# Performance work log

Measured on AMD Instinct MI355X. Metric: run time of the kernel, lower is better.

## Reference

```python
import jax, jax.numpy as jnp
import numpy as np

N, E = 50000, 800000
D_IN, D_E = 256, 64
H1, H2 = 128, 128
N_OUT = 64
LEAKY_SLOPE = 0.01  # torch.nn.LeakyReLU default
EPS = 1e-16         # PyG softmax denominator eps


def setup_inputs() -> dict:
    key = jax.random.key(0)
    ks = jax.random.split(key, 32)

    def w(k, shape, s=0.05):
        return jax.random.normal(k, shape, dtype=jnp.float32) * s

    inp = {
        "x_in": jax.random.normal(ks[0], (N, D_IN), dtype=jnp.float32),
        "edge_index": jax.random.randint(ks[1], (2, E), 0, N),
        "edge_atts": jax.random.normal(ks[2], (E, D_E), dtype=jnp.float32),
        # TransformerConv layer 1 (in=D_IN, out=H1, heads=1, beta=True, edge_dim=D_E)
        "Wq1": w(ks[3], (H1, D_IN)), "bq1": jnp.zeros((H1,), jnp.float32),
        "Wk1": w(ks[4], (H1, D_IN)), "bk1": jnp.zeros((H1,), jnp.float32),
        "Wv1": w(ks[5], (H1, D_IN)), "bv1": jnp.zeros((H1,), jnp.float32),
        "We1": w(ks[6], (H1, D_E)),                     # lin_edge (bias=False)
        "Wskip1": w(ks[7], (H1, D_IN)), "bskip1": jnp.zeros((H1,), jnp.float32),
        "Wbeta1": w(ks[8], (1, 3 * H1)),                # lin_beta (bias=False)
        # TransformerConv layer 2 (in=H1, out=H2)
        "Wq2": w(ks[9], (H2, H1)), "bq2": jnp.zeros((H2,), jnp.float32),
        "Wk2": w(ks[10], (H2, H1)), "bk2": jnp.zeros((H2,), jnp.float32),
        "Wv2": w(ks[11], (H2, H1)), "bv2": jnp.zeros((H2,), jnp.float32),
        "We2": w(ks[12], (H2, D_E)),
        "Wskip2": w(ks[13], (H2, H1)), "bskip2": jnp.zeros((H2,), jnp.float32),
        "Wbeta2": w(ks[14], (1, 3 * H2)),
        # output MLP: Linear(H1 + H2 -> N_OUT)
        "Wm": w(ks[15], (N_OUT, H1 + H2)), "bm": jnp.zeros((N_OUT,), jnp.float32),
    }
    return inp


def _transformer_conv(x, src, dst, edge_attr,
                      Wq, bq, Wk, bk, Wv, bv, We, Wskip, bskip, Wbeta, n_nodes):
    """PyG TransformerConv: heads=1, concat=True, beta=True, root_weight=True,
    dropout inactive (eval mode)."""
    d = Wq.shape[0]
    q = x @ Wq.T + bq                      # [N, d]
    k = x @ Wk.T + bk                      # [N, d]
    v = x @ Wv.T + bv                      # [N, d]
    e = edge_attr @ We.T                   # [E, d]
    k_e = k[src] + e                       # gather source keys + edge embedding
    v_e = v[src] + e                       # gather source values + edge embedding
    # attention score per edge
    score = jnp.einsum('ed,ed->e', q[dst], k_e) / jnp.sqrt(jnp.asarray(d, jnp.float32))
    # segment softmax over incoming edges of each destination node
    m = jax.ops.segment_max(score, dst, num_segments=n_nodes)
    m = jnp.where(jnp.isfinite(m), m, 0.0)
    ex = jnp.exp(score - m[dst])
    denom = jax.ops.segment_sum(ex, dst, num_segments=n_nodes) + EPS
    alpha = ex / denom[dst]                # [E]
    # scatter-add weighted messages
    out = jax.ops.segment_sum(alpha[:, None] * v_e, dst, num_segments=n_nodes)  # [N, d]
    # beta-gated skip connection
    x_r = x @ Wskip.T + bskip
    beta = jax.nn.sigmoid(jnp.concatenate([out, x_r, out - x_r], axis=1) @ Wbeta.T)  # [N, 1]
    return beta * x_r + (1.0 - beta) * out


def _leaky_relu(x):
    return jnp.where(x >= 0, x, LEAKY_SLOPE * x)


def reference(x_in, edge_index, edge_atts,
              Wq1, bq1, Wk1, bk1, Wv1, bv1, We1, Wskip1, bskip1, Wbeta1,
              Wq2, bq2, Wk2, bk2, Wv2, bv2, We2, Wskip2, bskip2, Wbeta2,
              Wm, bm):
    src, dst = edge_index[0], edge_index[1]
    n = x_in.shape[0]
    x1 = _leaky_relu(_transformer_conv(x_in, src, dst, edge_atts,
                                       Wq1, bq1, Wk1, bk1, Wv1, bv1, We1,
                                       Wskip1, bskip1, Wbeta1, n))
    x2 = _leaky_relu(_transformer_conv(x1, src, dst, edge_atts,
                                       Wq2, bq2, Wk2, bk2, Wv2, bv2, We2,
                                       Wskip2, bskip2, Wbeta2, n))
    out = jnp.concatenate([x1, x2], axis=1) @ Wm.T + bm   # [N, N_OUT]
    return out
```

## Files before the change

kernel.cpp:

```cpp
#include <hip/hip_runtime.h>
#include <hip/hip_bf16.h>
#include <math.h>


__global__ void count_deg(const int* __restrict__ dst, int* __restrict__ cnt, int E) {
    int e = blockIdx.x * blockDim.x + threadIdx.x;
    if (e < E) atomicAdd(&cnt[dst[e]], 1);
}

__global__ __launch_bounds__(1024) void scan_a(const int* __restrict__ cnt,
                                               int* __restrict__ out,
                                               int* __restrict__ partials, int N) {
    __shared__ int sh[1024];
    int tid = threadIdx.x;
    int gid = blockIdx.x * 1024 + tid;
    int v = (gid < N) ? cnt[gid] : 0;
    sh[tid] = v;
    for (int off = 1; off < 1024; off <<= 1) {
        __syncthreads();
        int add = (tid >= off) ? sh[tid - off] : 0;
        __syncthreads();
        sh[tid] += add;
    }
    __syncthreads();
    if (gid <= N) out[gid] = sh[tid] - v;
    if (tid == 1023) partials[blockIdx.x] = sh[1023];
}

__global__ void scan_b(int* __restrict__ partials, int nb) {
    if (threadIdx.x == 0 && blockIdx.x == 0) {
        int run = 0;
        for (int i = 0; i < nb; ++i) { int t = partials[i]; partials[i] = run; run += t; }
    }
}

__global__ __launch_bounds__(1024) void scan_c(int* __restrict__ out,
                                               const int* __restrict__ partials,
                                               int* __restrict__ fillb, int N) {
    int gid = blockIdx.x * 1024 + threadIdx.x;
    if (gid <= N) {
        int v = out[gid] + partials[blockIdx.x];
        out[gid] = v;
        fillb[gid] = v;
    }
}

__global__ void fill_edges(const int* __restrict__ src, const int* __restrict__ dst,
                           int* __restrict__ fillb, int2* __restrict__ esi, int E) {
    int e = blockIdx.x * blockDim.x + threadIdx.x;
    if (e < E) {
        int d = dst[e];
        int slot = atomicAdd(&fillb[d], 1);
        esi[slot] = make_int2(src[e], e);
    }
}

__global__ void transpose_we(const float* __restrict__ We, float* __restrict__ WeT) {
    int i = blockIdx.x * blockDim.x + threadIdx.x;
    if (i < 128 * 64) {
        int r = i >> 6, c = i & 63;
        WeT[c * 128 + r] = We[i];
    }
}

__global__ void build_wcat(const float* __restrict__ Wq, const float* __restrict__ Wk,
                           const float* __restrict__ Wv, const float* __restrict__ Ws,
                           const float* __restrict__ bq, const float* __restrict__ bk,
                           const float* __restrict__ bv, const float* __restrict__ bs,
                           float* __restrict__ Wcat, float* __restrict__ bcat,
                           int K, int kshift) {
    int i = blockIdx.x * blockDim.x + threadIdx.x;
    int total = 512 * K;
    if (i < total) {
        int r = i >> kshift;
        float v;
        if (r < 128)      v = Wq[i];
        else if (r < 256) v = Wk[i - (128 << kshift)];
        else if (r < 384) v = Wv[i - (256 << kshift)];
        else              v = Ws[i - (384 << kshift)];
        Wcat[i] = v;
    }
    if (i < 128) {
        bcat[i]       = bq[i];
        bcat[128 + i] = bk[i];
        bcat[256 + i] = bv[i];
        bcat[384 + i] = bs[i];
    }
}

#define TM 128
#define TO 64
#define TKK 16
__global__ __launch_bounds__(256) void gemm_nt2(const float* __restrict__ X, int ldx,
                                                const float* __restrict__ W,
                                                const float* __restrict__ bias,
                                                float* __restrict__ Out, int ldo,
                                                int Nrows, int K) {
    __shared__ float Xs[TKK][TM];
    __shared__ float Ws[TKK][TO];
    int n0 = blockIdx.x * TM, o0 = blockIdx.y * TO;
    int t  = threadIdx.x;
    int tx = t & 15, ty = t >> 4;
    int lr = t >> 1, lk = (t & 1) * 8;
    int wr = t >> 2, wk = (t & 3) * 4;
    float acc[8][4] = {};
    for (int k0 = 0; k0 < K; k0 += TKK) {
        int gr = n0 + lr;
        float4 x0 = make_float4(0.f, 0.f, 0.f, 0.f);
        float4 x1 = make_float4(0.f, 0.f, 0.f, 0.f);
        if (gr < Nrows) {
            const float* xp = &X[(size_t)gr * ldx + k0 + lk];
            x0 = *reinterpret_cast<const float4*>(xp);
            x1 = *reinterpret_cast<const float4*>(xp + 4);
        }
        Xs[lk + 0][lr] = x0.x; Xs[lk + 1][lr] = x0.y;
        Xs[lk + 2][lr] = x0.z; Xs[lk + 3][lr] = x0.w;
        Xs[lk + 4][lr] = x1.x; Xs[lk + 5][lr] = x1.y;
        Xs[lk + 6][lr] = x1.z; Xs[lk + 7][lr] = x1.w;
        float4 wv = *reinterpret_cast<const float4*>(&W[(size_t)(o0 + wr) * K + k0 + wk]);
        Ws[wk + 0][wr] = wv.x; Ws[wk + 1][wr] = wv.y;
        Ws[wk + 2][wr] = wv.z; Ws[wk + 3][wr] = wv.w;
        __syncthreads();
#pragma unroll
        for (int k = 0; k < TKK; ++k) {
            float4 a0 = *reinterpret_cast<const float4*>(&Xs[k][ty * 8]);
            float4 a1 = *reinterpret_cast<const float4*>(&Xs[k][ty * 8 + 4]);
            float4 b  = *reinterpret_cast<const float4*>(&Ws[k][tx * 4]);
            float av_[8] = {a0.x, a0.y, a0.z, a0.w, a1.x, a1.y, a1.z, a1.w};
            float bv_[4] = {b.x, b.y, b.z, b.w};
#pragma unroll
            for (int i = 0; i < 8; ++i)
#pragma unroll
                for (int j = 0; j < 4; ++j)
                    acc[i][j] = fmaf(av_[i], bv_[j], acc[i][j]);
        }
        __syncthreads();
    }
#pragma unroll
    for (int i = 0; i < 8; ++i) {
        int r = n0 + ty * 8 + i;
        if (r < Nrows) {
            int oc = o0 + tx * 4;
            float4 o4;
            o4.x = acc[i][0]; o4.y = acc[i][1]; o4.z = acc[i][2]; o4.w = acc[i][3];
            if (bias) {
                o4.x += bias[oc + 0]; o4.y += bias[oc + 1];
                o4.z += bias[oc + 2]; o4.w += bias[oc + 3];
            }
            *reinterpret_cast<float4*>(&Out[(size_t)r * ldo + oc]) = o4;
        }
    }
}

#define AW3 4
__global__ __launch_bounds__(256) void attn3(
    const int* __restrict__ row_ptr, const int2* __restrict__ esi,
    const float* __restrict__ QKVS, const float* __restrict__ QE,
    const float* __restrict__ Ae, float* __restrict__ Acc, int Nn) {
    int t = threadIdx.x;
    int wid = t >> 6, lane = t & 63;
    const float RS = 0.088388347648318447f;
    for (int n = blockIdx.x * AW3 + wid; n < Nn; n += gridDim.x * AW3) {
        int r0 = row_ptr[n], r1 = row_ptr[n + 1];
        const float* qrow = QKVS + (size_t)n * 512;
        float q0  = qrow[lane];
        float q1  = qrow[64 + lane];
        float qe0 = QE[(size_t)n * 64 + lane];
        float m = -1e30f, l = 0.f, av0 = 0.f, av1 = 0.f, aa = 0.f;
        for (int p = r0; p < r1; p += 8) {
            int pi[8];
#pragma unroll
            for (int i = 0; i < 8; ++i) pi[i] = (p + i < r1) ? p + i : r1 - 1;
            int2 se[8];
#pragma unroll
            for (int i = 0; i < 8; ++i) se[i] = esi[pi[i]];
            float k0v[8], k1v[8], a0v[8];
#pragma unroll
            for (int i = 0; i < 8; ++i) {
                const float* kr = QKVS + (size_t)se[i].x * 512 + 128;
                k0v[i] = kr[lane]; k1v[i] = kr[64 + lane];
            }
#pragma unroll
            for (int i = 0; i < 8; ++i) a0v[i] = Ae[(size_t)se[i].y * 64 + lane];
            float d[8];
#pragma unroll
            for (int i = 0; i < 8; ++i)
                d[i] = fmaf(q0, k0v[i], fmaf(q1, k1v[i], qe0 * a0v[i]));
#pragma unroll
            for (int off = 32; off; off >>= 1) {
#pragma unroll
                for (int i = 0; i < 8; ++i) d[i] += __shfl_xor(d[i], off, 64);
            }
            float v0v[8], v1v[8];
#pragma unroll
            for (int i = 0; i < 8; ++i) {
                const float* vr = QKVS + (size_t)se[i].x * 512 + 256;
                v0v[i] = vr[lane]; v1v[i] = vr[64 + lane];
            }
            float sc[8];
#pragma unroll
            for (int i = 0; i < 8; ++i) sc[i] = (p + i < r1) ? d[i] * RS : -1e30f;
            float bm = sc[0];
#pragma unroll
            for (int i = 1; i < 8; ++i) bm = fmaxf(bm, sc[i]);
            float mn = fmaxf(m, bm);
            float scale = __expf(m - mn);
            float w[8];
#pragma unroll
            for (int i = 0; i < 8; ++i) w[i] = __expf(sc[i] - mn);
            float ws = ((w[0] + w[1]) + (w[2] + w[3])) + ((w[4] + w[5]) + (w[6] + w[7]));
            l = fmaf(l, scale, ws);
            float s_aa = 0.f, s0 = 0.f, s1 = 0.f;
#pragma unroll
            for (int i = 0; i < 8; ++i) {
                s_aa = fmaf(w[i], a0v[i], s_aa);
                s0   = fmaf(w[i], v0v[i], s0);
                s1   = fmaf(w[i], v1v[i], s1);
            }
            aa  = fmaf(aa,  scale, s_aa);
            av0 = fmaf(av0, scale, s0);
            av1 = fmaf(av1, scale, s1);
            m = mn;
        }
        float inv = 1.0f / (l + 1e-16f);
        float* arow = Acc + (size_t)n * 192;
        arow[lane]       = av0 * inv;
        arow[64 + lane]  = av1 * inv;
        arow[128 + lane] = aa * inv;
    }
}

__global__ __launch_bounds__(256) void epilogue_k(
    const float* __restrict__ Acc, const float* __restrict__ QKVS,
    const float* __restrict__ WeT, const float* __restrict__ Wbeta,
    float* __restrict__ Xout, int ldo, int Nn) {
    __shared__ float WeS[64 * 128];
    __shared__ float wbA[128], wbB[128];
    int t = threadIdx.x;
    for (int i = t; i < 64 * 128; i += 256) WeS[i] = WeT[i];
    if (t < 128) {
        float w3 = Wbeta[256 + t];
        wbA[t] = Wbeta[t] + w3;
        wbB[t] = Wbeta[128 + t] - w3;
    }
    __syncthreads();
    int wid = t >> 6, lane = t & 63;
    for (int n = blockIdx.x * 4 + wid; n < Nn; n += gridDim.x * 4) {
        const float* ar = Acc + (size_t)n * 192;
        float out0 = ar[lane], out1 = ar[64 + lane], aa = ar[128 + lane];
#pragma unroll
        for (int j = 0; j < 64; ++j) {
            float aj = __shfl(aa, j, 64);
            out0 = fmaf(aj, WeS[j * 128 + lane], out0);
            out1 = fmaf(aj, WeS[j * 128 + 64 + lane], out1);
        }
        const float* qrow = QKVS + (size_t)n * 512;
        float xr0 = qrow[384 + lane], xr1 = qrow[448 + lane];
        float bp = wbA[lane] * out0 + wbA[64 + lane] * out1 +
                   wbB[lane] * xr0  + wbB[64 + lane] * xr1;
#pragma unroll
        for (int off = 32; off; off >>= 1) bp += __shfl_xor(bp, off, 64);
        float beta = 1.0f / (1.0f + __expf(-bp));
        float x0 = beta * xr0 + (1.0f - beta) * out0;
        float x1 = beta * xr1 + (1.0f - beta) * out1;
        x0 = (x0 >= 0.f) ? x0 : 0.01f * x0;
        x1 = (x1 >= 0.f) ? x1 : 0.01f * x1;
        Xout[(size_t)n * ldo + lane]      = x0;
        Xout[(size_t)n * ldo + 64 + lane] = x1;
    }
}

extern "C" void kernel_launch(void* const* d_in, const int* in_sizes, int n_in,
                              void* d_out, int out_size, void* d_ws, size_t ws_size,
                              hipStream_t stream) {
    const float* x_in  = (const float*)d_in[0];
    const int*   eidx  = (const int*)d_in[1];
    const float* eatt  = (const float*)d_in[2];
    const float* Wq1 = (const float*)d_in[3];  const float* bq1 = (const float*)d_in[4];
    const float* Wk1 = (const float*)d_in[5];  const float* bk1 = (const float*)d_in[6];
    const float* Wv1 = (const float*)d_in[7];  const float* bv1 = (const float*)d_in[8];
    const float* We1 = (const float*)d_in[9];
    const float* Wskip1 = (const float*)d_in[10]; const float* bskip1 = (const float*)d_in[11];
    const float* Wbeta1 = (const float*)d_in[12];
    const float* Wq2 = (const float*)d_in[13]; const float* bq2 = (const float*)d_in[14];
    const float* Wk2 = (const float*)d_in[15]; const float* bk2 = (const float*)d_in[16];
    const float* Wv2 = (const float*)d_in[17]; const float* bv2 = (const float*)d_in[18];
    const float* We2 = (const float*)d_in[19];
    const float* Wskip2 = (const float*)d_in[20]; const float* bskip2 = (const float*)d_in[21];
    const float* Wbeta2 = (const float*)d_in[22];
    const float* Wm  = (const float*)d_in[23]; const float* bm  = (const float*)d_in[24];

    const int N = in_sizes[0] / 256;
    const int E = in_sizes[1] / 2;
    const int* srcp = eidx;
    const int* dstp = eidx + E;

    char* p = (char*)d_ws;
    auto alloc = [&](size_t bytes) -> void* {
        void* r = (void*)p;
        p += (bytes + 255) & ~(size_t)255;
        return r;
    };
    int*   row_ptr  = (int*)alloc((size_t)(N + 1) * 4);
    int*   fillb    = (int*)alloc((size_t)(N + 1) * 4);
    int*   partials = (int*)alloc(256 * 4);
    int2*  esi      = (int2*)alloc((size_t)E * 8);
    float* QKVS = (float*)alloc((size_t)N * 512 * 4);
    float* QEb  = (float*)alloc((size_t)N * 64 * 4);
    float* Accb = (float*)alloc((size_t)N * 192 * 4);
    float* xcat = (float*)alloc((size_t)N * 256 * 4);
    float* WeT  = (float*)alloc((size_t)64 * 128 * 4);
    float* Wcat = (float*)alloc((size_t)512 * 256 * 4);
    float* bcat = (float*)alloc((size_t)512 * 4);

    hipMemsetAsync(fillb, 0, (size_t)(N + 1) * 4, stream);
    count_deg<<<(E + 255) / 256, 256, 0, stream>>>(dstp, fillb, E);
    int nScanBlocks = (N + 1 + 1023) / 1024;
    scan_a<<<nScanBlocks, 1024, 0, stream>>>(fillb, row_ptr, partials, N);
    scan_b<<<1, 1, 0, stream>>>(partials, nScanBlocks);
    scan_c<<<nScanBlocks, 1024, 0, stream>>>(row_ptr, partials, fillb, N);
    fill_edges<<<(E + 255) / 256, 256, 0, stream>>>(srcp, dstp, fillb, esi, E);

    dim3 blk(256);
    int gx = (N + TM - 1) / TM;

    build_wcat<<<(512 * 256 + 255) / 256, 256, 0, stream>>>(
        Wq1, Wk1, Wv1, Wskip1, bq1, bk1, bv1, bskip1, Wcat, bcat, 256, 8);
    transpose_we<<<(128 * 64 + 255) / 256, 256, 0, stream>>>(We1, WeT);
    gemm_nt2<<<dim3(gx, 8), blk, 0, stream>>>(x_in, 256, Wcat, bcat, QKVS, 512, N, 256);
    gemm_nt2<<<dim3(gx, 1), blk, 0, stream>>>(QKVS, 512, WeT, nullptr, QEb, 64, N, 128);
    attn3<<<2048, blk, 0, stream>>>(row_ptr, esi, QKVS, QEb, eatt, Accb, N);
    epilogue_k<<<1024, blk, 0, stream>>>(Accb, QKVS, WeT, Wbeta1, xcat, 256, N);

    build_wcat<<<(512 * 128 + 255) / 256, 256, 0, stream>>>(
        Wq2, Wk2, Wv2, Wskip2, bq2, bk2, bv2, bskip2, Wcat, bcat, 128, 7);
    transpose_we<<<(128 * 64 + 255) / 256, 256, 0, stream>>>(We2, WeT);
    gemm_nt2<<<dim3(gx, 8), blk, 0, stream>>>(xcat, 256, Wcat, bcat, QKVS, 512, N, 128);
    gemm_nt2<<<dim3(gx, 1), blk, 0, stream>>>(QKVS, 512, WeT, nullptr, QEb, 64, N, 128);
    attn3<<<2048, blk, 0, stream>>>(row_ptr, esi, QKVS, QEb, eatt, Accb, N);
    epilogue_k<<<1024, blk, 0, stream>>>(Accb, QKVS, WeT, Wbeta2, xcat + 128, 256, N);

    gemm_nt2<<<dim3(gx, 1), blk, 0, stream>>>(xcat, 256, Wm, bm, (float*)d_out, 64, N, 256);
}
```

Before: 1.145 ms.

## Use split-bf16 MFMA GEMMs and fold the q·We projection into the QKVS GEMM

Replaces the fp32 FMA tiled GEMM with an MFMA kernel that splits each operand into bf16 high and low planes and sums three products, keeping close to fp32 accuracy on matrix cores. It also precomputes We·Wq so the query-edge projection comes out of the main GEMM as 64 extra output columns, removing the separate second GEMM and its buffer. Layer outputs are written directly as bf16 hi/lo planes for the next GEMM. The cost is three MFMAs per tile instead of one, extra split kernels, and a small change in rounding.

```diff
diff --git a/kernel.cpp b/kernel.cpp
--- a/kernel.cpp
+++ b/kernel.cpp
@@ -2,6 +2,21 @@
 #include <hip/hip_bf16.h>
 #include <math.h>
 
+typedef unsigned short u16;
+typedef __attribute__((ext_vector_type(8))) short bf16x8;
+typedef __attribute__((ext_vector_type(4))) float f32x4;
+
+__device__ inline u16 f2bf(float x) {
+    unsigned u = __float_as_uint(x);
+    unsigned r = u + 0x7fff + ((u >> 16) & 1);
+    return (u16)(r >> 16);
+}
+__device__ inline float bf2f(u16 h) { return __uint_as_float(((unsigned)h) << 16); }
+__device__ inline void bsplit(float x, u16& h, u16& l) {
+    h = f2bf(x);
+    float r = x - bf2f(h);
+    l = f2bf(r);
+}
 
 __global__ void count_deg(const int* __restrict__ dst, int* __restrict__ cnt, int E) {
     int e = blockIdx.x * blockDim.x + threadIdx.x;
@@ -63,21 +78,40 @@
     }
 }
 
+__global__ __launch_bounds__(256) void wcomb_k(const float* __restrict__ We,
+                                               const float* __restrict__ Wq,
+                                               const float* __restrict__ bq,
+                                               float* __restrict__ WcT,
+                                               float* __restrict__ bqe, int Din) {
+    int o = blockIdx.x;
+    int d = threadIdx.x;
+    float s = 0.f, sb = 0.f;
+    for (int h = 0; h < 128; ++h) {
+        float w = We[h * 64 + o];
+        if (d < Din) s = fmaf(w, Wq[h * Din + d], s);
+        sb = fmaf(w, bq[h], sb);
+    }
+    if (d < Din) WcT[o * Din + d] = s;
+    if (d == 0) bqe[o] = sb;
+}
+
 __global__ void build_wcat(const float* __restrict__ Wq, const float* __restrict__ Wk,
                            const float* __restrict__ Wv, const float* __restrict__ Ws,
+                           const float* __restrict__ Wc,
                            const float* __restrict__ bq, const float* __restrict__ bk,
                            const float* __restrict__ bv, const float* __restrict__ bs,
+                           const float* __restrict__ bqe,
                            float* __restrict__ Wcat, float* __restrict__ bcat,
                            int K, int kshift) {
     int i = blockIdx.x * blockDim.x + threadIdx.x;
-    int total = 512 * K;
-    if (i < total) {
+    if (i < 576 * K) {
         int r = i >> kshift;
         float v;
         if (r < 128)      v = Wq[i];
         else if (r < 256) v = Wk[i - (128 << kshift)];
         else if (r < 384) v = Wv[i - (256 << kshift)];
-        else              v = Ws[i - (384 << kshift)];
+        else if (r < 512) v = Ws[i - (384 << kshift)];
+        else              v = Wc[i - (512 << kshift)];
         Wcat[i] = v;
     }
     if (i < 128) {
@@ -86,86 +120,121 @@
         bcat[256 + i] = bv[i];
         bcat[384 + i] = bs[i];
     }
-}
-
-#define TM 128
-#define TO 64
-#define TKK 16
-__global__ __launch_bounds__(256) void gemm_nt2(const float* __restrict__ X, int ldx,
-                                                const float* __restrict__ W,
-                                                const float* __restrict__ bias,
-                                                float* __restrict__ Out, int ldo,
-                                                int Nrows, int K) {
-    __shared__ float Xs[TKK][TM];
-    __shared__ float Ws[TKK][TO];
-    int n0 = blockIdx.x * TM, o0 = blockIdx.y * TO;
-    int t  = threadIdx.x;
-    int tx = t & 15, ty = t >> 4;
-    int lr = t >> 1, lk = (t & 1) * 8;
-    int wr = t >> 2, wk = (t & 3) * 4;
-    float acc[8][4] = {};
-    for (int k0 = 0; k0 < K; k0 += TKK) {
-        int gr = n0 + lr;
-        float4 x0 = make_float4(0.f, 0.f, 0.f, 0.f);
-        float4 x1 = make_float4(0.f, 0.f, 0.f, 0.f);
-        if (gr < Nrows) {
-            const float* xp = &X[(size_t)gr * ldx + k0 + lk];
-            x0 = *reinterpret_cast<const float4*>(xp);
-            x1 = *reinterpret_cast<const float4*>(xp + 4);
-        }
-        Xs[lk + 0][lr] = x0.x; Xs[lk + 1][lr] = x0.y;
-        Xs[lk + 2][lr] = x0.z; Xs[lk + 3][lr] = x0.w;
-        Xs[lk + 4][lr] = x1.x; Xs[lk + 5][lr] = x1.y;
-        Xs[lk + 6][lr] = x1.z; Xs[lk + 7][lr] = x1.w;
-        float4 wv = *reinterpret_cast<const float4*>(&W[(size_t)(o0 + wr) * K + k0 + wk]);
-        Ws[wk + 0][wr] = wv.x; Ws[wk + 1][wr] = wv.y;
-        Ws[wk + 2][wr] = wv.z; Ws[wk + 3][wr] = wv.w;
+    if (i < 64) bcat[512 + i] = bqe[i];
+}
+
+__global__ void split_planes(const float* __restrict__ src, u16* __restrict__ hi,
+                             u16* __restrict__ lo, int n4) {
+    int i = (blockIdx.x * blockDim.x + threadIdx.x) * 4;
+    if (i < n4) {
+        float4 v = *reinterpret_cast<const float4*>(&src[i]);
+        u16 h0, h1, h2, h3, l0, l1, l2, l3;
+        bsplit(v.x, h0, l0); bsplit(v.y, h1, l1);
+        bsplit(v.z, h2, l2); bsplit(v.w, h3, l3);
+        ushort4 hv = make_ushort4(h0, h1, h2, h3);
+        ushort4 lv = make_ushort4(l0, l1, l2, l3);
+        *reinterpret_cast<ushort4*>(&hi[i]) = hv;
+        *reinterpret_cast<ushort4*>(&lo[i]) = lv;
+    }
+}
+
+#define BM 128
+#define BO 64
+#define BKX 64
+#define LSTR 72
+__global__ __launch_bounds__(256) void gemm_mfma(
+    const u16* __restrict__ XH, const u16* __restrict__ XL, int ldx,
+    const u16* __restrict__ WH, const u16* __restrict__ WL,
+    const float* __restrict__ bias, float* __restrict__ Out, int ldo,
+    int Nrows, int K) {
+    __shared__ __align__(16) u16 XsH[BM * LSTR];
+    __shared__ __align__(16) u16 XsL[BM * LSTR];
+    __shared__ __align__(16) u16 WsH[BO * LSTR];
+    __shared__ __align__(16) u16 WsL[BO * LSTR];
+    int n0 = blockIdx.x * BM, o0 = blockIdx.y * BO;
+    int t = threadIdx.x, wid = t >> 6, lane = t & 63;
+    int xr = t >> 1, xk = (t & 1) * 32;
+    int wr = t >> 2, wk = (t & 3) * 16;
+    bool xok = (n0 + xr) < Nrows;
+    const u16* xh = XH + (size_t)(n0 + xr) * ldx + xk;
+    const u16* xl = XL + (size_t)(n0 + xr) * ldx + xk;
+    const u16* wh = WH + (size_t)(o0 + wr) * K + wk;
+    const u16* wl = WL + (size_t)(o0 + wr) * K + wk;
+    f32x4 acc[2][4] = {};
+    for (int k0 = 0; k0 < K; k0 += BKX) {
+#pragma unroll
+        for (int j = 0; j < 4; ++j) {
+            bf16x8 vh = {0, 0, 0, 0, 0, 0, 0, 0};
+            bf16x8 vl = {0, 0, 0, 0, 0, 0, 0, 0};
+            if (xok) {
+                vh = *reinterpret_cast<const bf16x8*>(xh + k0 + 8 * j);
+                vl = *reinterpret_cast<const bf16x8*>(xl + k0 + 8 * j);
+            }
+            *reinterpret_cast<bf16x8*>(&XsH[xr * LSTR + xk + 8 * j]) = vh;
+            *reinterpret_cast<bf16x8*>(&XsL[xr * LSTR + xk + 8 * j]) = vl;
+        }
+#pragma unroll
+        for (int j = 0; j < 2; ++j) {
+            *reinterpret_cast<bf16x8*>(&WsH[wr * LSTR + wk + 8 * j]) =
+                *reinterpret_cast<const bf16x8*>(wh + k0 + 8 * j);
+            *reinterpret_cast<bf16x8*>(&WsL[wr * LSTR + wk + 8 * j]) =
+                *reinterpret_cast<const bf16x8*>(wl + k0 + 8 * j);
+        }
         __syncthreads();
 #pragma unroll
-        for (int k = 0; k < TKK; ++k) {
-            float4 a0 = *reinterpret_cast<const float4*>(&Xs[k][ty * 8]);
-            float4 a1 = *reinterpret_cast<const float4*>(&Xs[k][ty * 8 + 4]);
-            float4 b  = *reinterpret_cast<const float4*>(&Ws[k][tx * 4]);
-            float av_[8] = {a0.x, a0.y, a0.z, a0.w, a1.x, a1.y, a1.z, a1.w};
-            float bv_[4] = {b.x, b.y, b.z, b.w};
-#pragma unroll
-            for (int i = 0; i < 8; ++i)
-#pragma unroll
-                for (int j = 0; j < 4; ++j)
-                    acc[i][j] = fmaf(av_[i], bv_[j], acc[i][j]);
+        for (int kc = 0; kc < 2; ++kc) {
+            int kf = kc * 32 + (lane >> 4) * 8;
+            int ar = wid * 32 + (lane & 15);
+            bf16x8 aH0 = *reinterpret_cast<const bf16x8*>(&XsH[ar * LSTR + kf]);
+            bf16x8 aH1 = *reinterpret_cast<const bf16x8*>(&XsH[(ar + 16) * LSTR + kf]);
+            bf16x8 aL0 = *reinterpret_cast<const bf16x8*>(&XsL[ar * LSTR + kf]);
+            bf16x8 aL1 = *reinterpret_cast<const bf16x8*>(&XsL[(ar + 16) * LSTR + kf]);
+#pragma unroll
+            for (int c = 0; c < 4; ++c) {
+                int br = c * 16 + (lane & 15);
+                bf16x8 bH = *reinterpret_cast<const bf16x8*>(&WsH[br * LSTR + kf]);
+                bf16x8 bL = *reinterpret_cast<const bf16x8*>(&WsL[br * LSTR + kf]);
+                acc[0][c] = __builtin_amdgcn_mfma_f32_16x16x32_bf16(aH0, bH, acc[0][c], 0, 0, 0);
+                acc[1][c] = __builtin_amdgcn_mfma_f32_16x16x32_bf16(aH1, bH, acc[1][c], 0, 0, 0);
+                acc[0][c] = __builtin_amdgcn_mfma_f32_16x16x32_bf16(aH0, bL, acc[0][c], 0, 0, 0);
+                acc[1][c] = __builtin_amdgcn_mfma_f32_16x16x32_bf16(aH1, bL, acc[1][c], 0, 0, 0);
+                acc[0][c] = __builtin_amdgcn_mfma_f32_16x16x32_bf16(aL0, bH, acc[0][c], 0, 0, 0);
+                acc[1][c] = __builtin_amdgcn_mfma_f32_16x16x32_bf16(aL1, bH, acc[1][c], 0, 0, 0);
+            }
         }
         __syncthreads();
     }
 #pragma unroll
-    for (int i = 0; i < 8; ++i) {
-        int r = n0 + ty * 8 + i;
-        if (r < Nrows) {
-            int oc = o0 + tx * 4;
-            float4 o4;
-            o4.x = acc[i][0]; o4.y = acc[i][1]; o4.z = acc[i][2]; o4.w = acc[i][3];
-            if (bias) {
-                o4.x += bias[oc + 0]; o4.y += bias[oc + 1];
-                o4.z += bias[oc + 2]; o4.w += bias[oc + 3];
-            }
-            *reinterpret_cast<float4*>(&Out[(size_t)r * ldo + oc]) = o4;
+    for (int c = 0; c < 4; ++c) {
+        int col = o0 + c * 16 + (lane & 15);
+        float bb = bias ? bias[col] : 0.f;
+#pragma unroll
+        for (int r = 0; r < 2; ++r) {
+            int rb = n0 + wid * 32 + r * 16 + (lane >> 4) * 4;
+#pragma unroll
+            for (int q = 0; q < 4; ++q) {
+                int row = rb + q;
+                if (row < Nrows) Out[(size_t)row * ldo + col] = acc[r][c][q] + bb;
+            }
         }
     }
 }
 
 #define AW3 4
+#define LD6 576
 __global__ __launch_bounds__(256) void attn3(
     const int* __restrict__ row_ptr, const int2* __restrict__ esi,
-    const float* __restrict__ QKVS, const float* __restrict__ QE,
-    const float* __restrict__ Ae, float* __restrict__ Acc, int Nn) {
+    const float* __restrict__ QKVS, const float* __restrict__ Ae,
+    float* __restrict__ Acc, int Nn) {
     int t = threadIdx.x;
     int wid = t >> 6, lane = t & 63;
     const float RS = 0.088388347648318447f;
     for (int n = blockIdx.x * AW3 + wid; n < Nn; n += gridDim.x * AW3) {
         int r0 = row_ptr[n], r1 = row_ptr[n + 1];
-        const float* qrow = QKVS + (size_t)n * 512;
+        const float* qrow = QKVS + (size_t)n * LD6;
         float q0  = qrow[lane];
         float q1  = qrow[64 + lane];
-        float qe0 = QE[(size_t)n * 64 + lane];
+        float qe0 = qrow[512 + lane];
         float m = -1e30f, l = 0.f, av0 = 0.f, av1 = 0.f, aa = 0.f;
         for (int p = r0; p < r1; p += 8) {
             int pi[8];
@@ -177,7 +246,7 @@
             float k0v[8], k1v[8], a0v[8];
 #pragma unroll
             for (int i = 0; i < 8; ++i) {
-                const float* kr = QKVS + (size_t)se[i].x * 512 + 128;
+                const float* kr = QKVS + (size_t)se[i].x * LD6 + 128;
                 k0v[i] = kr[lane]; k1v[i] = kr[64 + lane];
             }
 #pragma unroll
@@ -194,7 +263,7 @@
             float v0v[8], v1v[8];
 #pragma unroll
             for (int i = 0; i < 8; ++i) {
-                const float* vr = QKVS + (size_t)se[i].x * 512 + 256;
+                const float* vr = QKVS + (size_t)se[i].x * LD6 + 256;
                 v0v[i] = vr[lane]; v1v[i] = vr[64 + lane];
             }
             float sc[8];
@@ -233,7 +302,7 @@
 __global__ __launch_bounds__(256) void epilogue_k(
     const float* __restrict__ Acc, const float* __restrict__ QKVS,
     const float* __restrict__ WeT, const float* __restrict__ Wbeta,
-    float* __restrict__ Xout, int ldo, int Nn) {
+    u16* __restrict__ XoH, u16* __restrict__ XoL, int coff, int Nn) {
     __shared__ float WeS[64 * 128];
     __shared__ float wbA[128], wbB[128];
     int t = threadIdx.x;
@@ -254,7 +323,7 @@
             out0 = fmaf(aj, WeS[j * 128 + lane], out0);
             out1 = fmaf(aj, WeS[j * 128 + 64 + lane], out1);
         }
-        const float* qrow = QKVS + (size_t)n * 512;
+        const float* qrow = QKVS + (size_t)n * LD6;
         float xr0 = qrow[384 + lane], xr1 = qrow[448 + lane];
         float bp = wbA[lane] * out0 + wbA[64 + lane] * out1 +
                    wbB[lane] * xr0  + wbB[64 + lane] * xr1;
@@ -265,8 +334,10 @@
         float x1 = beta * xr1 + (1.0f - beta) * out1;
         x0 = (x0 >= 0.f) ? x0 : 0.01f * x0;
         x1 = (x1 >= 0.f) ? x1 : 0.01f * x1;
-        Xout[(size_t)n * ldo + lane]      = x0;
-        Xout[(size_t)n * ldo + 64 + lane] = x1;
+        u16 h, l;
+        size_t base = (size_t)n * 256 + coff;
+        bsplit(x0, h, l); XoH[base + lane] = h;      XoL[base + lane] = l;
+        bsplit(x1, h, l); XoH[base + 64 + lane] = h; XoL[base + 64 + lane] = l;
     }
 }
 
@@ -305,13 +376,19 @@
     int*   fillb    = (int*)alloc((size_t)(N + 1) * 4);
     int*   partials = (int*)alloc(256 * 4);
     int2*  esi      = (int2*)alloc((size_t)E * 8);
-    float* QKVS = (float*)alloc((size_t)N * 512 * 4);
-    float* QEb  = (float*)alloc((size_t)N * 64 * 4);
+    float* QKVS = (float*)alloc((size_t)N * 576 * 4);
     float* Accb = (float*)alloc((size_t)N * 192 * 4);
-    float* xcat = (float*)alloc((size_t)N * 256 * 4);
+    u16*   XpH  = (u16*)alloc((size_t)N * 256 * 2);
+    u16*   XpL  = (u16*)alloc((size_t)N * 256 * 2);
     float* WeT  = (float*)alloc((size_t)64 * 128 * 4);
-    float* Wcat = (float*)alloc((size_t)512 * 256 * 4);
-    float* bcat = (float*)alloc((size_t)512 * 4);
+    float* Wcat = (float*)alloc((size_t)576 * 256 * 4);
+    u16*   WcH  = (u16*)alloc((size_t)576 * 256 * 2);
+    u16*   WcL  = (u16*)alloc((size_t)576 * 256 * 2);
+    float* WcombT = (float*)alloc((size_t)64 * 256 * 4);
+    float* bcat = (float*)alloc(576 * 4);
+    float* bqe  = (float*)alloc(64 * 4);
+    u16*   WmH  = (u16*)alloc((size_t)64 * 256 * 2);
+    u16*   WmL  = (u16*)alloc((size_t)64 * 256 * 2);
 
     hipMemsetAsync(fillb, 0, (size_t)(N + 1) * 4, stream);
     count_deg<<<(E + 255) / 256, 256, 0, stream>>>(dstp, fillb, E);
@@ -322,23 +399,31 @@
     fill_edges<<<(E + 255) / 256, 256, 0, stream>>>(srcp, dstp, fillb, esi, E);
 
     dim3 blk(256);
-    int gx = (N + TM - 1) / TM;
-
-    build_wcat<<<(512 * 256 + 255) / 256, 256, 0, stream>>>(
-        Wq1, Wk1, Wv1, Wskip1, bq1, bk1, bv1, bskip1, Wcat, bcat, 256, 8);
+    int gmx = (N + BM - 1) / BM;
+
+    split_planes<<<(N * 256 / 4 + 255) / 256, 256, 0, stream>>>(x_in, XpH, XpL, N * 256);
+
+    wcomb_k<<<64, 256, 0, stream>>>(We1, Wq1, bq1, WcombT, bqe, 256);
+    build_wcat<<<(576 * 256 + 255) / 256, 256, 0, stream>>>(
+        Wq1, Wk1, Wv1, Wskip1, WcombT, bq1, bk1, bv1, bskip1, bqe, Wcat, bcat, 256, 8);
+    split_planes<<<(576 * 256 / 4 + 255) / 256, 256, 0, stream>>>(Wcat, WcH, WcL, 576 * 256);
     transpose_we<<<(128 * 64 + 255) / 256, 256, 0, stream>>>(We1, WeT);
-    gemm_nt2<<<dim3(gx, 8), blk, 0, stream>>>(x_in, 256, Wcat, bcat, QKVS, 512, N, 256);
-    gemm_nt2<<<dim3(gx, 1), blk, 0, stream>>>(QKVS, 512, WeT, nullptr, QEb, 64, N, 128);
-    attn3<<<2048, blk, 0, stream>>>(row_ptr, esi, QKVS, QEb, eatt, Accb, N);
-    epilogue_k<<<1024, blk, 0, stream>>>(Accb, QKVS, WeT, Wbeta1, xcat, 256, N);
-
-    build_wcat<<<(512 * 128 + 255) / 256, 256, 0, stream>>>(
-        Wq2, Wk2, Wv2, Wskip2, bq2, bk2, bv2, bskip2, Wcat, bcat, 128, 7);
+    gemm_mfma<<<dim3(gmx, 9), blk, 0, stream>>>(XpH, XpL, 256, WcH, WcL, bcat,
+                                                QKVS, 576, N, 256);
+    attn3<<<2048, blk, 0, stream>>>(row_ptr, esi, QKVS, eatt, Accb, N);
+    epilogue_k<<<1024, blk, 0, stream>>>(Accb, QKVS, WeT, Wbeta1, XpH, XpL, 0, N);
+
+    wcomb_k<<<64, 256, 0, stream>>>(We2, Wq2, bq2, WcombT, bqe, 128);
+    build_wcat<<<(576 * 128 + 255) / 256, 256, 0, stream>>>(
+        Wq2, Wk2, Wv2, Wskip2, WcombT, bq2, bk2, bv2, bskip2, bqe, Wcat, bcat, 128, 7);
+    split_planes<<<(576 * 128 / 4 + 255) / 256, 256, 0, stream>>>(Wcat, WcH, WcL, 576 * 128);
     transpose_we<<<(128 * 64 + 255) / 256, 256, 0, stream>>>(We2, WeT);
-    gemm_nt2<<<dim3(gx, 8), blk, 0, stream>>>(xcat, 256, Wcat, bcat, QKVS, 512, N, 128);
-    gemm_nt2<<<dim3(gx, 1), blk, 0, stream>>>(QKVS, 512, WeT, nullptr, QEb, 64, N, 128);
-    attn3<<<2048, blk, 0, stream>>>(row_ptr, esi, QKVS, QEb, eatt, Accb, N);
-    epilogue_k<<<1024, blk, 0, stream>>>(Accb, QKVS, WeT, Wbeta2, xcat + 128, 256, N);
-
-    gemm_nt2<<<dim3(gx, 1), blk, 0, stream>>>(xcat, 256, Wm, bm, (float*)d_out, 64, N, 256);
-}
+    gemm_mfma<<<dim3(gmx, 9), blk, 0, stream>>>(XpH, XpL, 256, WcH, WcL, bcat,
+                                                QKVS, 576, N, 128);
+    attn3<<<2048, blk, 0, stream>>>(row_ptr, esi, QKVS, eatt, Accb, N);
+    epilogue_k<<<1024, blk, 0, stream>>>(Accb, QKVS, WeT, Wbeta2, XpH, XpL, 128, N);
+
+    split_planes<<<(64 * 256 / 4 + 255) / 256, 256, 0, stream>>>(Wm, WmH, WmL, 64 * 256);
+    gemm_mfma<<<dim3(gmx, 1), blk, 0, stream>>>(XpH, XpL, 256, WmH, WmL, bm,
+                                                (float*)d_out, 64, N, 256);
+}
```

Result: no change. 1.158 ms (+1.1%).
